# Optimization experiments

Hardware: AMD Instinct MI355X
Metric: run time of the kernel (lower is better)

The kernel has to match this reference:

```python
import jax, jax.numpy as jnp
import numpy as np

B, L = 256, 32768

def _avg_pool1d(x, k, p):
    # count_include_pad=True avg pool via prefix sums: O(L) instead of O(L*k)
    xp = jnp.pad(x, ((0, 0), (0, 0), (p, p)))
    cs = jnp.cumsum(xp, axis=-1)
    cs = jnp.pad(cs, ((0, 0), (0, 0), (1, 0)))  # leading zero for window diff
    return (cs[..., k:] - cs[..., :-k]) / k

def setup_inputs() -> dict:
    key = jax.random.key(0)
    x = jax.random.normal(key, (B, L), dtype=jnp.float32)
    return {"x": x}

def reference(x):
    x = x[:, None, :]  # [B, 1, L]
    # log(max(1, 1+x)) and log(max(1, 1-x)): cat-with-ones + max == clamp at 1
    a = jnp.log(jnp.maximum(1.0, 1.0 + x))
    b = jnp.log(jnp.maximum(1.0, 1.0 - x))
    a0 = _avg_pool1d(a, 3, 1)
    a5 = _avg_pool1d(a, 199, 99)
    b0 = _avg_pool1d(b, 3, 1)
    b5 = _avg_pool1d(b, 199, 99)
    return jnp.concatenate([a0 - a5, a0, b0 - b5, b0], axis=1)  # [B, 4, L]
```

## Files before the change

### kernel.cpp

```cpp
#include <hip/hip_runtime.h>

#define B_DIM 256
#define L_DIM 32768
#define CHUNK 2048
#define HALO  100
#define NTOT  (CHUNK + 2*HALO)
#define T     256
#define EPT   9

__global__ __launch_bounds__(T) void pool_feat_kernel(const float* __restrict__ x,
                                                      float* __restrict__ out) {
    const int row    = blockIdx.y;
    const int chunk0 = blockIdx.x * CHUNK;
    const int tid    = threadIdx.x;

    __shared__ float sA[NTOT];
    __shared__ float sB[NTOT];
    __shared__ float waveA[4];
    __shared__ float waveB[4];

    const float* xr = x + (size_t)row * L_DIM;

    for (int j = tid; j < NTOT; j += T) {
        int col = chunk0 - HALO + j;
        float v = (col >= 0 && col < L_DIM) ? xr[col] : 0.0f;
        sA[j] = logf(fmaxf(1.0f, 1.0f + v));
        sB[j] = logf(fmaxf(1.0f, 1.0f - v));
    }
    __syncthreads();

    const int s0 = tid * EPT;
    const int s1 = min(NTOT, s0 + EPT);
    float runA = 0.0f, runB = 0.0f;
    for (int j = s0; j < s1; ++j) {
        runA += sA[j]; sA[j] = runA;
        runB += sB[j]; sB[j] = runB;
    }

    float vA = runA, vB = runB;
    const int lane = tid & 63;
    const int wid  = tid >> 6;
    #pragma unroll
    for (int d = 1; d < 64; d <<= 1) {
        float uA = __shfl_up(vA, d);
        float uB = __shfl_up(vB, d);
        if (lane >= d) { vA += uA; vB += uB; }
    }
    if (lane == 63) { waveA[wid] = vA; waveB[wid] = vB; }
    __syncthreads();
    float offA = vA - runA;
    float offB = vB - runB;
    for (int w = 0; w < wid; ++w) { offA += waveA[w]; offB += waveB[w]; }

    for (int j = s0; j < s1; ++j) { sA[j] += offA; sB[j] += offB; }
    __syncthreads();

    const float inv3   = 1.0f / 3.0f;
    const float inv199 = 1.0f / 199.0f;
    const size_t outbase = (size_t)row * 4u * L_DIM;
    for (int i = tid; i < CHUNK; i += T) {
        const int col = chunk0 + i;
        float sum199a = sA[i + 199] - sA[i];
        float sum3a   = sA[i + 101] - sA[i + 98];
        float sum199b = sB[i + 199] - sB[i];
        float sum3b   = sB[i + 101] - sB[i + 98];
        float a0 = sum3a * inv3, a5 = sum199a * inv199;
        float b0 = sum3b * inv3, b5 = sum199b * inv199;
        out[outbase + 0u * L_DIM + col] = a0 - a5;
        out[outbase + 1u * L_DIM + col] = a0;
        out[outbase + 2u * L_DIM + col] = b0 - b5;
        out[outbase + 3u * L_DIM + col] = b0;
    }
}

extern "C" void kernel_launch(void* const* d_in, const int* in_sizes, int n_in,
                              void* d_out, int out_size, void* d_ws, size_t ws_size,
                              hipStream_t stream) {
    const float* x = (const float*)d_in[0];
    float* out = (float*)d_out;
    dim3 grid(L_DIM / CHUNK, B_DIM);
    pool_feat_kernel<<<grid, dim3(T), 0, stream>>>(x, out);
}
```

Measured before the change: 35.38 us.

## Vectorize loads/stores, move log into scan, keep scan partials in registers

Global loads of x and output stores become float4 vector accesses. The log transform moves from the load loop into the per-thread scan and uses the fast __logf intrinsic. Raw x is staged once in shared memory and the scan partials stay in registers, which removes a shared-memory read-modify-write pass. The wave-offset loop is unrolled. The approximate log may change accuracy slightly, and stride-9 shared reads can cause bank conflicts.

```diff
diff --git a/kernel.cpp b/kernel.cpp
--- a/kernel.cpp
+++ b/kernel.cpp
@@ -5,6 +5,7 @@
 #define CHUNK 2048
 #define HALO  100
 #define NTOT  (CHUNK + 2*HALO)
+#define NG    (NTOT/4)
 #define T     256
 #define EPT   9
 
@@ -14,27 +15,38 @@
     const int chunk0 = blockIdx.x * CHUNK;
     const int tid    = threadIdx.x;
 
-    __shared__ float sA[NTOT];
-    __shared__ float sB[NTOT];
+    __shared__ __align__(16) float sA[NTOT];
+    __shared__ __align__(16) float sB[NTOT];
     __shared__ float waveA[4];
     __shared__ float waveB[4];
 
     const float* xr = x + (size_t)row * L_DIM;
 
-    for (int j = tid; j < NTOT; j += T) {
-        int col = chunk0 - HALO + j;
-        float v = (col >= 0 && col < L_DIM) ? xr[col] : 0.0f;
-        sA[j] = logf(fmaxf(1.0f, 1.0f + v));
-        sB[j] = logf(fmaxf(1.0f, 1.0f - v));
+    for (int g = tid; g < NG; g += T) {
+        const int c = chunk0 - HALO + 4 * g;
+        float4 v;
+        if (c >= 0 && c + 3 < L_DIM) {
+            v = *reinterpret_cast<const float4*>(xr + c);
+        } else {
+            v.x = (c + 0 >= 0 && c + 0 < L_DIM) ? xr[c + 0] : 0.0f;
+            v.y = (c + 1 >= 0 && c + 1 < L_DIM) ? xr[c + 1] : 0.0f;
+            v.z = (c + 2 >= 0 && c + 2 < L_DIM) ? xr[c + 2] : 0.0f;
+            v.w = (c + 3 >= 0 && c + 3 < L_DIM) ? xr[c + 3] : 0.0f;
+        }
+        *reinterpret_cast<float4*>(&sA[4 * g]) = v;
     }
     __syncthreads();
 
     const int s0 = tid * EPT;
-    const int s1 = min(NTOT, s0 + EPT);
+    float ra[EPT], rb[EPT];
     float runA = 0.0f, runB = 0.0f;
-    for (int j = s0; j < s1; ++j) {
-        runA += sA[j]; sA[j] = runA;
-        runB += sB[j]; sB[j] = runB;
+    #pragma unroll
+    for (int j = 0; j < EPT; ++j) {
+        const int idx = s0 + j;
+        const float v = (idx < NTOT) ? sA[idx] : 0.0f;
+        runA += __logf(fmaxf(1.0f, 1.0f + v));
+        runB += __logf(fmaxf(1.0f, 1.0f - v));
+        ra[j] = runA; rb[j] = runB;
     }
 
     float vA = runA, vB = runB;
@@ -50,26 +62,43 @@
     __syncthreads();
     float offA = vA - runA;
     float offB = vB - runB;
-    for (int w = 0; w < wid; ++w) { offA += waveA[w]; offB += waveB[w]; }
+    #pragma unroll
+    for (int w = 0; w < 3; ++w) {
+        if (w < wid) { offA += waveA[w]; offB += waveB[w]; }
+    }
 
-    for (int j = s0; j < s1; ++j) { sA[j] += offA; sB[j] += offB; }
+    #pragma unroll
+    for (int j = 0; j < EPT; ++j) {
+        const int idx = s0 + j;
+        if (idx < NTOT) { sA[idx] = ra[j] + offA; sB[idx] = rb[j] + offB; }
+    }
     __syncthreads();
 
     const float inv3   = 1.0f / 3.0f;
     const float inv199 = 1.0f / 199.0f;
-    const size_t outbase = (size_t)row * 4u * L_DIM;
-    for (int i = tid; i < CHUNK; i += T) {
-        const int col = chunk0 + i;
-        float sum199a = sA[i + 199] - sA[i];
-        float sum3a   = sA[i + 101] - sA[i + 98];
-        float sum199b = sB[i + 199] - sB[i];
-        float sum3b   = sB[i + 101] - sB[i + 98];
-        float a0 = sum3a * inv3, a5 = sum199a * inv199;
-        float b0 = sum3b * inv3, b5 = sum199b * inv199;
-        out[outbase + 0u * L_DIM + col] = a0 - a5;
-        out[outbase + 1u * L_DIM + col] = a0;
-        out[outbase + 2u * L_DIM + col] = b0 - b5;
-        out[outbase + 3u * L_DIM + col] = b0;
+    float* ob = out + (size_t)row * 4u * L_DIM + chunk0;
+    #pragma unroll
+    for (int it = 0; it < CHUNK / (4 * T); ++it) {
+        const int i0 = 4 * (tid + it * T);
+        float4 r0, r1, r2, r3;
+        #pragma unroll
+        for (int u = 0; u < 4; ++u) {
+            const int i = i0 + u;
+            float s199a = sA[i + 199] - sA[i];
+            float s3a   = sA[i + 101] - sA[i + 98];
+            float s199b = sB[i + 199] - sB[i];
+            float s3b   = sB[i + 101] - sB[i + 98];
+            float a0 = s3a * inv3, a5 = s199a * inv199;
+            float b0 = s3b * inv3, b5 = s199b * inv199;
+            reinterpret_cast<float*>(&r0)[u] = a0 - a5;
+            reinterpret_cast<float*>(&r1)[u] = a0;
+            reinterpret_cast<float*>(&r2)[u] = b0 - b5;
+            reinterpret_cast<float*>(&r3)[u] = b0;
+        }
+        *reinterpret_cast<float4*>(ob + 0 * (size_t)L_DIM + i0) = r0;
+        *reinterpret_cast<float4*>(ob + 1 * (size_t)L_DIM + i0) = r1;
+        *reinterpret_cast<float4*>(ob + 2 * (size_t)L_DIM + i0) = r2;
+        *reinterpret_cast<float4*>(ob + 3 * (size_t)L_DIM + i0) = r3;
     }
 }
 
```

New measurement: 33.58 us. -5.1%, faster.
